# Performance work log

Measured on AMD Instinct MI355X. Metric: run time of the kernel, lower is better.

## Reference

```python
import jax, jax.numpy as jnp
import numpy as np

N = 50000      # nodes
E = 1_600_000  # edges (before self-loops)
G = 100        # graphs in batch
IN = 16        # in_channels
H1, C1 = 4, 32 # gat1 heads, per-head channels
H2, C2 = 1, 32 # gat2 heads, per-head channels
NEG_SLOPE = 0.2


def setup_inputs() -> dict:
    key = jax.random.key(0)
    ks = jax.random.split(key, 16)
    s = 0.1
    return {
        "x": jax.random.normal(ks[0], (N, IN), jnp.float32),
        "edge_index": jax.random.randint(ks[1], (2, E), 0, N, dtype=jnp.int64),
        "batch": jnp.sort(jax.random.randint(ks[2], (N,), 0, G, dtype=jnp.int64)),
        # GATConv 1: lin (no bias), att_src/att_dst, output bias (concat -> H1*C1)
        "W1": jax.random.normal(ks[3], (IN, H1 * C1), jnp.float32) * s,
        "att_src1": jax.random.normal(ks[4], (H1, C1), jnp.float32) * s,
        "att_dst1": jax.random.normal(ks[5], (H1, C1), jnp.float32) * s,
        "b1": jnp.zeros((H1 * C1,), jnp.float32),
        # GATConv 2
        "W2": jax.random.normal(ks[6], (H1 * C1, H2 * C2), jnp.float32) * s,
        "att_src2": jax.random.normal(ks[7], (H2, C2), jnp.float32) * s,
        "att_dst2": jax.random.normal(ks[8], (H2, C2), jnp.float32) * s,
        "b2": jnp.zeros((H2 * C2,), jnp.float32),
        # MLP head: Linear(32,64) -> ReLU -> Linear(64,1)
        "Wh1": jax.random.normal(ks[9], (C2, 64), jnp.float32) * s,
        "bh1": jnp.zeros((64,), jnp.float32),
        "Wh2": jax.random.normal(ks[10], (64, 1), jnp.float32) * s,
        "bh2": jnp.zeros((1,), jnp.float32),
    }


def gat_conv(x, src, dst, W, a_src, a_dst, bias, heads, ch):
    """PyG GATConv (self-loops already included in src/dst), eval mode."""
    n = x.shape[0]
    h = (x @ W).reshape(n, heads, ch)                 # [N,H,C]
    # per-node attention logits, then gather per edge
    a_s = jnp.einsum('nhc,hc->nh', h, a_src)          # [N,H]
    a_d = jnp.einsum('nhc,hc->nh', h, a_dst)
    e = jax.nn.leaky_relu(a_s[src] + a_d[dst], NEG_SLOPE)  # [E,H]
    # segment softmax over incoming edges of each destination node
    m = jax.ops.segment_max(e, dst, num_segments=n)   # [N,H]
    ex = jnp.exp(e - m[dst])
    denom = jax.ops.segment_sum(ex, dst, num_segments=n)
    alpha = ex / (denom[dst] + 1e-16)                 # [E,H]
    # weighted scatter-aggregate of source features
    out = jax.ops.segment_sum(alpha[:, :, None] * h[src], dst, num_segments=n)
    return out.reshape(n, heads * ch) + bias


def reference(x, edge_index, batch, W1, att_src1, att_dst1, b1,
              W2, att_src2, att_dst2, b2, Wh1, bh1, Wh2, bh2):
    n = x.shape[0]
    loops = jnp.arange(n, dtype=edge_index.dtype)
    src = jnp.concatenate([edge_index[0], loops])
    dst = jnp.concatenate([edge_index[1], loops])

    h = jax.nn.elu(gat_conv(x, src, dst, W1, att_src1, att_dst1, b1, H1, C1))
    h = jax.nn.elu(gat_conv(h, src, dst, W2, att_src2, att_dst2, b2, H2, C2))

    # global mean pool by graph id
    sums = jax.ops.segment_sum(h, batch, num_segments=G)          # [G,C2]
    cnts = jax.ops.segment_sum(jnp.ones((n,), h.dtype), batch, num_segments=G)
    pooled = sums / jnp.maximum(cnts, 1.0)[:, None]

    out = jax.nn.relu(pooled @ Wh1 + bh1) @ Wh2 + bh2             # [G,1]
    return out
```

## Files before the change

### kernel.cpp

```cpp
#include <hip/hip_runtime.h>
#include <hip/hip_fp16.h>
#include <math.h>

#define IN_CH 16
#define HC1 128
#define NH1 4
#define C2 32
#define HID 64
#define NEG 0.2f
#define CAP 10240
#define CHUNK 4096

__device__ __forceinline__ float lrelu_exp_fast(float z) {
    float lr = fmaxf(z, NEG * z);
    return __expf(lr);
}

__device__ __forceinline__ void fma_mix_lo(float& acc, int hpack, float w) {
    asm("v_fma_mix_f32 %0, %1, %2, %0 op_sel:[0,0,0] op_sel_hi:[1,0,0]"
        : "+v"(acc) : "v"(hpack), "v"(w));
}
__device__ __forceinline__ void fma_mix_hi(float& acc, int hpack, float w) {
    asm("v_fma_mix_f32 %0, %1, %2, %0 op_sel:[1,0,0] op_sel_hi:[1,0,0]"
        : "+v"(acc) : "v"(hpack), "v"(w));
}

__global__ void k_front(const int* __restrict__ ei, int E, int N, int nchunk,
                        int* __restrict__ cursors, int* __restrict__ buckets,
                        const float* __restrict__ x, const float2* __restrict__ W1v,
                        const float2* __restrict__ att_s2, const float2* __restrict__ att_d2,
                        __half2* __restrict__ h1h, float* __restrict__ as1, float* __restrict__ ad1) {
    int bid = blockIdx.x;
    if (bid < nchunk) {
        __shared__ int cnt[256];
        __shared__ int base[256];
        __shared__ int pos[256];
        int t = threadIdx.x;
        int c0 = bid * CHUNK;
        int M = E + N;
        cnt[t] = 0;
        pos[t] = 0;
        __syncthreads();
        int srcv[16], dstv[16];
#pragma unroll
        for (int k = 0; k < 16; ++k) {
            int i = c0 + k * 256 + t;
            int s = -1, d = -1;
            if (i < M) {
                if (i < E) { s = ei[i]; d = ei[E + i]; }
                else       { s = d = i - E; }
                atomicAdd(&cnt[d >> 8], 1);
            }
            srcv[k] = s; dstv[k] = d;
        }
        __syncthreads();
        if (cnt[t] > 0) base[t] = atomicAdd(&cursors[t], cnt[t]);
        __syncthreads();
#pragma unroll
        for (int k = 0; k < 16; ++k) {
            int d = dstv[k];
            if (d >= 0) {
                int b = d >> 8;
                int p = base[b] + atomicAdd(&pos[b], 1);
                buckets[b * CAP + p] = (srcv[k] << 8) | (d & 255);
            }
        }
    } else {
        int wave = threadIdx.x >> 6;
        int lane = threadIdx.x & 63;
        int n = (bid - nchunk) * 4 + wave;
        if (n >= N) return;
        float xv = x[n * IN_CH + (lane & 15)];
        float ax = 0.f, ay = 0.f;
#pragma unroll
        for (int k = 0; k < IN_CH; ++k) {
            float xk = __shfl(xv, k, 16);
            float2 w = W1v[k * 64 + lane];
            ax += xk * w.x;
            ay += xk * w.y;
        }
        h1h[(size_t)n * 64 + lane] = __floats2half2_rn(ax, ay);
        float2 s2 = att_s2[lane], d2 = att_d2[lane];
        float vs = ax * s2.x + ay * s2.y;
        float vd = ax * d2.x + ay * d2.y;
#pragma unroll
        for (int o = 1; o < 16; o <<= 1) {
            vs += __shfl_xor(vs, o, 64);
            vd += __shfl_xor(vd, o, 64);
        }
        if ((lane & 15) == 0) {
            as1[n * NH1 + (lane >> 4)] = vs;
            ad1[n * NH1 + (lane >> 4)] = vd;
        }
    }
}

__global__ void k_build(const int* __restrict__ buckets, const int* __restrict__ cursors,
                        int N, int M,
                        int* __restrict__ offsets, int* __restrict__ elist) {
    __shared__ int sc[256];
    __shared__ int deg[256];
    __shared__ int cur[256];
    int b = blockIdx.x, t = threadIdx.x;
    int cv = cursors[t];
    sc[t] = cv;
    __syncthreads();
    for (int o = 1; o < 256; o <<= 1) {
        int a = (t >= o) ? sc[t - o] : 0;
        __syncthreads();
        sc[t] += a;
        __syncthreads();
    }
    int cnt = cursors[b];
    int gbase = sc[b] - cnt;
    int n0 = b << 8;
    const int* bk = buckets + b * CAP;
    deg[t] = 0;
    if (b == 0 && t == 0) offsets[N] = M;
    __syncthreads();
    for (int i = t; i < cnt; i += 256) atomicAdd(&deg[bk[i] & 255], 1);
    __syncthreads();
    int v = deg[t];
    sc[t] = v;
    __syncthreads();
    for (int o = 1; o < 256; o <<= 1) {
        int a = (t >= o) ? sc[t - o] : 0;
        __syncthreads();
        sc[t] += a;
        __syncthreads();
    }
    int excl = sc[t] - v;
    cur[t] = excl;
    if (n0 + t < N) offsets[n0 + t] = gbase + excl;
    __syncthreads();
    for (int i = t; i < cnt; i += 256) {
        int e = bk[i];
        int p = atomicAdd(&cur[e & 255], 1);
        elist[gbase + p] = e >> 8;
    }
}

__global__ void k_agg1(const int* __restrict__ offsets, const int* __restrict__ elist,
                       const char* __restrict__ as1b, const float* __restrict__ ad1,
                       const char* __restrict__ h1b, const float* __restrict__ b1,
                       int N, float4* __restrict__ out1q) {
    int wave = threadIdx.x >> 6;
    int lane = threadIdx.x & 63;
    int n = blockIdx.x * 4 + wave;
    if (n >= N) return;
    int slot = lane >> 4, chunk = lane & 15, head = chunk >> 2;
    int lo = offsets[n], hi = offsets[n + 1];
    float adh = ad1[n * NH1 + head];
    unsigned coff = (unsigned)(chunk << 4);
    unsigned hoff = (unsigned)(head << 2);
    float acc[8];
#pragma unroll
    for (int j = 0; j < 8; ++j) acc[j] = 0.f;
    float sumw = 0.f;
    for (int e0 = lo; e0 < hi; e0 += 16) {
        unsigned s[4]; bool ok[4]; float z[4]; float4 v[4]; float w[4];
#pragma unroll
        for (int u = 0; u < 4; ++u) {
            int ee = e0 + 4 * u + slot;
            ok[u] = ee < hi;
            s[u] = (unsigned)elist[ok[u] ? ee : lo];
        }
#pragma unroll
        for (int u = 0; u < 4; ++u) {
            z[u] = *(const float*)(as1b + (s[u] * 16u + hoff));
            v[u] = *(const float4*)(h1b + (s[u] * 256u + coff));
        }
#pragma unroll
        for (int u = 0; u < 4; ++u)
            w[u] = ok[u] ? lrelu_exp_fast(z[u] + adh) : 0.f;
#pragma unroll
        for (int u = 0; u < 4; ++u) {
            const int* hp = (const int*)&v[u];
            fma_mix_lo(acc[0], hp[0], w[u]); fma_mix_hi(acc[1], hp[0], w[u]);
            fma_mix_lo(acc[2], hp[1], w[u]); fma_mix_hi(acc[3], hp[1], w[u]);
            fma_mix_lo(acc[4], hp[2], w[u]); fma_mix_hi(acc[5], hp[2], w[u]);
            fma_mix_lo(acc[6], hp[3], w[u]); fma_mix_hi(acc[7], hp[3], w[u]);
            sumw += w[u];
        }
    }
#pragma unroll
    for (int j = 0; j < 8; ++j) {
        acc[j] += __shfl_xor(acc[j], 16, 64);
        acc[j] += __shfl_xor(acc[j], 32, 64);
    }
    sumw += __shfl_xor(sumw, 16, 64);
    sumw += __shfl_xor(sumw, 32, 64);
    if (slot == 0) {
        float inv = 1.f / (sumw + 1e-16f);
        float4 ba = ((const float4*)b1)[2 * chunk];
        float4 bb = ((const float4*)b1)[2 * chunk + 1];
        float o[8];
        o[0] = acc[0] * inv + ba.x; o[1] = acc[1] * inv + ba.y;
        o[2] = acc[2] * inv + ba.z; o[3] = acc[3] * inv + ba.w;
        o[4] = acc[4] * inv + bb.x; o[5] = acc[5] * inv + bb.y;
        o[6] = acc[6] * inv + bb.z; o[7] = acc[7] * inv + bb.w;
#pragma unroll
        for (int j = 0; j < 8; ++j) o[j] = o[j] > 0.f ? o[j] : expm1f(o[j]);
        float4 pk;
        __half2* ph = (__half2*)&pk;
        ph[0] = __floats2half2_rn(o[0], o[1]);
        ph[1] = __floats2half2_rn(o[2], o[3]);
        ph[2] = __floats2half2_rn(o[4], o[5]);
        ph[3] = __floats2half2_rn(o[6], o[7]);
        out1q[(size_t)n * 16 + chunk] = pk;
    }
}

#define TN 64
__global__ void k_lin2(const __half2* __restrict__ out1h, const float* __restrict__ W2,
                       const float* __restrict__ att_s, const float* __restrict__ att_d,
                       int N, __half2* __restrict__ h2h, float* __restrict__ as2, float* __restrict__ ad2) {
    __shared__ float sx[TN][HC1 + 1];
    __shared__ float sw[HC1][C2];
    int t = threadIdx.x;
    int base = blockIdx.x * TN;
    int lim = (N - base) * HC1;
    for (int i = t * 4; i < HC1 * C2; i += 1024) {
        float4 v = *(const float4*)(W2 + i);
        sw[i >> 5][i & 31] = v.x;
        sw[i >> 5][(i & 31) + 1] = v.y;
        sw[i >> 5][(i & 31) + 2] = v.z;
        sw[i >> 5][(i & 31) + 3] = v.w;
    }
    for (int i = t * 4; i < TN * HC1; i += 1024) {
        float2 a = make_float2(0.f, 0.f), b = make_float2(0.f, 0.f);
        if (i < lim) {
            size_t idx = ((size_t)base * HC1 + i) >> 1;
            a = __half22float2(out1h[idx]);
            b = __half22float2(out1h[idx + 1]);
        }
        int nn = i >> 7, kk = i & 127;
        sx[nn][kk] = a.x; sx[nn][kk + 1] = a.y; sx[nn][kk + 2] = b.x; sx[nn][kk + 3] = b.y;
    }
    __syncthreads();
    int nloc = t >> 2;
    int c0 = (t & 3) * 8;
    float acc[8];
#pragma unroll
    for (int j = 0; j < 8; ++j) acc[j] = 0.f;
#pragma unroll 4
    for (int k = 0; k < HC1; ++k) {
        float xv = sx[nloc][k];
        float4 wa = *(float4*)&sw[k][c0];
        float4 wb = *(float4*)&sw[k][c0 + 4];
        acc[0] += xv * wa.x; acc[1] += xv * wa.y; acc[2] += xv * wa.z; acc[3] += xv * wa.w;
        acc[4] += xv * wb.x; acc[5] += xv * wb.y; acc[6] += xv * wb.z; acc[7] += xv * wb.w;
    }
    int n = base + nloc;
    if (n < N) {
#pragma unroll
        for (int j = 0; j < 4; ++j)
            h2h[(size_t)n * 16 + (c0 >> 1) + j] = __floats2half2_rn(acc[2 * j], acc[2 * j + 1]);
        float ps = 0.f, pd = 0.f;
#pragma unroll
        for (int j = 0; j < 8; ++j) {
            ps += acc[j] * att_s[c0 + j];
            pd += acc[j] * att_d[c0 + j];
        }
        ps += __shfl_down(ps, 1, 64); ps += __shfl_down(ps, 2, 64);
        pd += __shfl_down(pd, 1, 64); pd += __shfl_down(pd, 2, 64);
        if ((t & 3) == 0) { as2[n] = ps; ad2[n] = pd; }
    }
}

__global__ void k_agg2(const int* __restrict__ offsets, const int* __restrict__ elist,
                       const char* __restrict__ as2b, const float* __restrict__ ad2,
                       const char* __restrict__ h2b, const float* __restrict__ b2,
                       int N, float* __restrict__ out2) {
    int wave = threadIdx.x >> 6;
    int lane = threadIdx.x & 63;
    int n = blockIdx.x * 4 + wave;
    if (n >= N) return;
    int slot = lane >> 2, chunk = lane & 3;
    int lo = offsets[n], hi = offsets[n + 1];
    float ad = ad2[n];
    unsigned coff = (unsigned)(chunk << 4);
    float acc[8];
#pragma unroll
    for (int j = 0; j < 8; ++j) acc[j] = 0.f;
    float sumw = 0.f;
    for (int e0 = lo; e0 < hi; e0 += 32) {
        unsigned s[2]; bool ok[2]; float z[2]; float4 v[2]; float w[2];
#pragma unroll
        for (int u = 0; u < 2; ++u) {
            int ee = e0 + 16 * u + slot;
            ok[u] = ee < hi;
            s[u] = (unsigned)elist[ok[u] ? ee : lo];
        }
#pragma unroll
        for (int u = 0; u < 2; ++u) {
            z[u] = *(const float*)(as2b + (s[u] * 4u));
            v[u] = *(const float4*)(h2b + (s[u] * 64u + coff));
        }
#pragma unroll
        for (int u = 0; u < 2; ++u)
            w[u] = ok[u] ? lrelu_exp_fast(z[u] + ad) : 0.f;
#pragma unroll
        for (int u = 0; u < 2; ++u) {
            const int* hp = (const int*)&v[u];
            fma_mix_lo(acc[0], hp[0], w[u]); fma_mix_hi(acc[1], hp[0], w[u]);
            fma_mix_lo(acc[2], hp[1], w[u]); fma_mix_hi(acc[3], hp[1], w[u]);
            fma_mix_lo(acc[4], hp[2], w[u]); fma_mix_hi(acc[5], hp[2], w[u]);
            fma_mix_lo(acc[6], hp[3], w[u]); fma_mix_hi(acc[7], hp[3], w[u]);
            sumw += w[u];
        }
    }
#pragma unroll
    for (int j = 0; j < 8; ++j) {
        acc[j] += __shfl_xor(acc[j], 4, 64);
        acc[j] += __shfl_xor(acc[j], 8, 64);
        acc[j] += __shfl_xor(acc[j], 16, 64);
        acc[j] += __shfl_xor(acc[j], 32, 64);
    }
    sumw += __shfl_xor(sumw, 4, 64);
    sumw += __shfl_xor(sumw, 8, 64);
    sumw += __shfl_xor(sumw, 16, 64);
    sumw += __shfl_xor(sumw, 32, 64);
    if (slot == 0) {
        float inv = 1.f / (sumw + 1e-16f);
        float4 ba = ((const float4*)b2)[2 * chunk];
        float4 bb = ((const float4*)b2)[2 * chunk + 1];
        float o[8];
        o[0] = acc[0] * inv + ba.x; o[1] = acc[1] * inv + ba.y;
        o[2] = acc[2] * inv + ba.z; o[3] = acc[3] * inv + ba.w;
        o[4] = acc[4] * inv + bb.x; o[5] = acc[5] * inv + bb.y;
        o[6] = acc[6] * inv + bb.z; o[7] = acc[7] * inv + bb.w;
#pragma unroll
        for (int j = 0; j < 8; ++j) o[j] = o[j] > 0.f ? o[j] : expm1f(o[j]);
        float* dst = out2 + (size_t)n * C2 + 8 * chunk;
        *(float4*)dst = make_float4(o[0], o[1], o[2], o[3]);
        *(float4*)(dst + 4) = make_float4(o[4], o[5], o[6], o[7]);
    }
}

__global__ void k_pool(const float* __restrict__ out2, const int* __restrict__ batch,
                       int N, const float* __restrict__ Wh1, const float* __restrict__ bh1,
                       const float* __restrict__ Wh2, const float* __restrict__ bh2,
                       float* __restrict__ out) {
    int g = blockIdx.x;
    int t = threadIdx.x;
    __shared__ int sb[2];
    __shared__ float pooled[C2];
    __shared__ float red[256];
    if (t < 2) {
        int target = g + t;
        int lo = 0, hi = N;
        while (lo < hi) { int mid = (lo + hi) >> 1; if (batch[mid] < target) lo = mid + 1; else hi = mid; }
        sb[t] = lo;
    }
    __syncthreads();
    int lo = sb[0], hi = sb[1];
    int c = t & 31, grp = t >> 5;
    float part = 0.f;
    for (int n = lo + grp; n < hi; n += 8) part += out2[n * C2 + c];
    red[t] = part;
    __syncthreads();
    if (t < 128) red[t] += red[t + 128];
    __syncthreads();
    if (t < 64) red[t] += red[t + 64];
    __syncthreads();
    if (t < 32) {
        red[t] += red[t + 32];
        float cnt = (float)(hi - lo);
        pooled[t] = red[t] / fmaxf(cnt, 1.f);
    }
    __syncthreads();
    float hval = 0.f;
    if (t < HID) {
        float a = bh1[t];
#pragma unroll
        for (int cc = 0; cc < C2; ++cc) a += pooled[cc] * Wh1[cc * HID + t];
        hval = fmaxf(a, 0.f) * Wh2[t];
    }
    if (t < 64) {
        for (int o = 32; o > 0; o >>= 1) hval += __shfl_down(hval, o, 64);
        if (t == 0) out[g] = hval + bh2[0];
    }
}

extern "C" void kernel_launch(void* const* d_in, const int* in_sizes, int n_in,
                              void* d_out, int out_size, void* d_ws, size_t ws_size,
                              hipStream_t stream) {
    const float* x    = (const float*)d_in[0];
    const int*   ei   = (const int*)d_in[1];
    const int*   batch= (const int*)d_in[2];
    const float* W1   = (const float*)d_in[3];
    const float* aS1  = (const float*)d_in[4];
    const float* aD1  = (const float*)d_in[5];
    const float* b1   = (const float*)d_in[6];
    const float* W2   = (const float*)d_in[7];
    const float* aS2  = (const float*)d_in[8];
    const float* aD2  = (const float*)d_in[9];
    const float* b2   = (const float*)d_in[10];
    const float* Wh1  = (const float*)d_in[11];
    const float* bh1  = (const float*)d_in[12];
    const float* Wh2  = (const float*)d_in[13];
    const float* bh2  = (const float*)d_in[14];
    float* out = (float*)d_out;

    int N = in_sizes[2];
    int E = in_sizes[1] / 2;
    int M = E + N;
    int G = out_size;
    int nbk = (N + 255) >> 8;
    int nchunk = (M + CHUNK - 1) / CHUNK;
    int nlin = (N + 3) / 4;

    char* p = (char*)d_ws;
    auto alloc = [&](size_t bytes) -> void* {
        void* r = (void*)p;
        p += (bytes + 255) & ~(size_t)255;
        return r;
    };
    __half2* h1h   = (__half2*)alloc((size_t)N * 64 * 4);
    __half2* out1h = (__half2*)alloc((size_t)N * 64 * 4);
    __half2* h2h   = (__half2*)alloc((size_t)N * 16 * 4);
    float* as1     = (float*)alloc((size_t)N * NH1 * 4);
    float* ad1     = (float*)alloc((size_t)N * NH1 * 4);
    float* as2     = (float*)alloc((size_t)N * 4);
    float* ad2     = (float*)alloc((size_t)N * 4);
    float* out2    = (float*)alloc((size_t)N * C2 * 4);
    int*   offsets = (int*)alloc((size_t)(N + 1) * 4);
    int*   elist   = (int*)alloc((size_t)M * 4);
    int*   cursors = (int*)alloc(256 * 4);
    int*   buckets = (int*)alloc((size_t)nbk * CAP * 4);

    hipMemsetAsync(cursors, 0, 256 * 4, stream);
    k_front<<<nchunk + nlin, 256, 0, stream>>>(ei, E, N, nchunk, cursors, buckets,
                                               x, (const float2*)W1, (const float2*)aS1,
                                               (const float2*)aD1, h1h, as1, ad1);
    k_build<<<nbk, 256, 0, stream>>>(buckets, cursors, N, M, offsets, elist);
    k_agg1<<<(N + 3) / 4, 256, 0, stream>>>(offsets, elist, (const char*)as1, ad1,
                                            (const char*)h1h, b1, N, (float4*)out1h);
    k_lin2<<<(N + TN - 1) / TN, 256, 0, stream>>>(out1h, W2, aS2, aD2, N, h2h, as2, ad2);
    k_agg2<<<(N + 3) / 4, 256, 0, stream>>>(offsets, elist, (const char*)as2, ad2,
                                            (const char*)h2h, b2, N, out2);
    k_pool<<<G, 256, 0, stream>>>(out2, batch, N, Wh1, bh1, Wh2, bh2, out);
}
```

Before: 279.1 us.

## Store layer-1 features head-major and split aggregation blocks per head

```diff
diff --git a/kernel.cpp b/kernel.cpp
--- a/kernel.cpp
+++ b/kernel.cpp
@@ -29,7 +29,7 @@
                         int* __restrict__ cursors, int* __restrict__ buckets,
                         const float* __restrict__ x, const float2* __restrict__ W1v,
                         const float2* __restrict__ att_s2, const float2* __restrict__ att_d2,
-                        __half2* __restrict__ h1h, float* __restrict__ as1, float* __restrict__ ad1) {
+                        __half2* __restrict__ h1s, float* __restrict__ as1s, float* __restrict__ ad1s) {
     int bid = blockIdx.x;
     if (bid < nchunk) {
         __shared__ int cnt[256];
@@ -79,7 +79,8 @@
             ax += xk * w.x;
             ay += xk * w.y;
         }
-        h1h[(size_t)n * 64 + lane] = __floats2half2_rn(ax, ay);
+        int head = lane >> 4;
+        h1s[((size_t)head * N + n) * 16 + (lane & 15)] = __floats2half2_rn(ax, ay);
         float2 s2 = att_s2[lane], d2 = att_d2[lane];
         float vs = ax * s2.x + ay * s2.y;
         float vd = ax * d2.x + ay * d2.y;
@@ -89,8 +90,8 @@
             vd += __shfl_xor(vd, o, 64);
         }
         if ((lane & 15) == 0) {
-            as1[n * NH1 + (lane >> 4)] = vs;
-            ad1[n * NH1 + (lane >> 4)] = vd;
+            as1s[(size_t)head * N + n] = vs;
+            ad1s[(size_t)head * N + n] = vd;
         }
     }
 }
@@ -141,40 +142,44 @@
 }
 
 __global__ void k_agg1(const int* __restrict__ offsets, const int* __restrict__ elist,
-                       const char* __restrict__ as1b, const float* __restrict__ ad1,
+                       const char* __restrict__ as1b, const float* __restrict__ ad1s,
                        const char* __restrict__ h1b, const float* __restrict__ b1,
-                       int N, float4* __restrict__ out1q) {
+                       int N, int nblk, char* __restrict__ out1b) {
+    int bid = blockIdx.x;
+    unsigned head = (unsigned)bid / (unsigned)nblk;
+    int nb = bid - (int)head * nblk;
     int wave = threadIdx.x >> 6;
     int lane = threadIdx.x & 63;
-    int n = blockIdx.x * 4 + wave;
+    int n = nb * 4 + wave;
     if (n >= N) return;
-    int slot = lane >> 4, chunk = lane & 15, head = chunk >> 2;
+    int slot = lane >> 2, c4 = lane & 3;
     int lo = offsets[n], hi = offsets[n + 1];
-    float adh = ad1[n * NH1 + head];
-    unsigned coff = (unsigned)(chunk << 4);
-    unsigned hoff = (unsigned)(head << 2);
+    const char* ab = as1b + (size_t)head * N * 4;
+    const char* hb = h1b + (size_t)head * N * 64;
+    float adh = ad1s[(size_t)head * N + n];
+    unsigned coff = (unsigned)(c4 << 4);
     float acc[8];
 #pragma unroll
     for (int j = 0; j < 8; ++j) acc[j] = 0.f;
     float sumw = 0.f;
-    for (int e0 = lo; e0 < hi; e0 += 16) {
-        unsigned s[4]; bool ok[4]; float z[4]; float4 v[4]; float w[4];
-#pragma unroll
-        for (int u = 0; u < 4; ++u) {
-            int ee = e0 + 4 * u + slot;
+    for (int e0 = lo; e0 < hi; e0 += 32) {
+        unsigned s[2]; bool ok[2]; float z[2]; float4 v[2]; float w[2];
+#pragma unroll
+        for (int u = 0; u < 2; ++u) {
+            int ee = e0 + 16 * u + slot;
             ok[u] = ee < hi;
             s[u] = (unsigned)elist[ok[u] ? ee : lo];
         }
 #pragma unroll
-        for (int u = 0; u < 4; ++u) {
-            z[u] = *(const float*)(as1b + (s[u] * 16u + hoff));
-            v[u] = *(const float4*)(h1b + (s[u] * 256u + coff));
-        }
-#pragma unroll
-        for (int u = 0; u < 4; ++u)
+        for (int u = 0; u < 2; ++u) {
+            z[u] = *(const float*)(ab + (s[u] * 4u));
+            v[u] = *(const float4*)(hb + (s[u] * 64u + coff));
+        }
+#pragma unroll
+        for (int u = 0; u < 2; ++u)
             w[u] = ok[u] ? lrelu_exp_fast(z[u] + adh) : 0.f;
 #pragma unroll
-        for (int u = 0; u < 4; ++u) {
+        for (int u = 0; u < 2; ++u) {
             const int* hp = (const int*)&v[u];
             fma_mix_lo(acc[0], hp[0], w[u]); fma_mix_hi(acc[1], hp[0], w[u]);
             fma_mix_lo(acc[2], hp[1], w[u]); fma_mix_hi(acc[3], hp[1], w[u]);
@@ -185,29 +190,31 @@
     }
 #pragma unroll
     for (int j = 0; j < 8; ++j) {
+        acc[j] += __shfl_xor(acc[j], 4, 64);
+        acc[j] += __shfl_xor(acc[j], 8, 64);
         acc[j] += __shfl_xor(acc[j], 16, 64);
         acc[j] += __shfl_xor(acc[j], 32, 64);
     }
+    sumw += __shfl_xor(sumw, 4, 64);
+    sumw += __shfl_xor(sumw, 8, 64);
     sumw += __shfl_xor(sumw, 16, 64);
     sumw += __shfl_xor(sumw, 32, 64);
     if (slot == 0) {
         float inv = 1.f / (sumw + 1e-16f);
-        float4 ba = ((const float4*)b1)[2 * chunk];
-        float4 bb = ((const float4*)b1)[2 * chunk + 1];
+        const float* bp = b1 + head * 32 + c4 * 8;
         float o[8];
-        o[0] = acc[0] * inv + ba.x; o[1] = acc[1] * inv + ba.y;
-        o[2] = acc[2] * inv + ba.z; o[3] = acc[3] * inv + ba.w;
-        o[4] = acc[4] * inv + bb.x; o[5] = acc[5] * inv + bb.y;
-        o[6] = acc[6] * inv + bb.z; o[7] = acc[7] * inv + bb.w;
-#pragma unroll
-        for (int j = 0; j < 8; ++j) o[j] = o[j] > 0.f ? o[j] : expm1f(o[j]);
+#pragma unroll
+        for (int j = 0; j < 8; ++j) {
+            float val = acc[j] * inv + bp[j];
+            o[j] = val > 0.f ? val : expm1f(val);
+        }
         float4 pk;
         __half2* ph = (__half2*)&pk;
         ph[0] = __floats2half2_rn(o[0], o[1]);
         ph[1] = __floats2half2_rn(o[2], o[3]);
         ph[2] = __floats2half2_rn(o[4], o[5]);
         ph[3] = __floats2half2_rn(o[6], o[7]);
-        out1q[(size_t)n * 16 + chunk] = pk;
+        *(float4*)(out1b + ((size_t)n * 256 + head * 64 + coff)) = pk;
     }
 }
 
@@ -410,6 +417,7 @@
     int nbk = (N + 255) >> 8;
     int nchunk = (M + CHUNK - 1) / CHUNK;
     int nlin = (N + 3) / 4;
+    int nblk = (N + 3) / 4;
 
     char* p = (char*)d_ws;
     auto alloc = [&](size_t bytes) -> void* {
@@ -417,11 +425,11 @@
         p += (bytes + 255) & ~(size_t)255;
         return r;
     };
-    __half2* h1h   = (__half2*)alloc((size_t)N * 64 * 4);
+    __half2* h1s   = (__half2*)alloc((size_t)N * 64 * 4);
     __half2* out1h = (__half2*)alloc((size_t)N * 64 * 4);
     __half2* h2h   = (__half2*)alloc((size_t)N * 16 * 4);
-    float* as1     = (float*)alloc((size_t)N * NH1 * 4);
-    float* ad1     = (float*)alloc((size_t)N * NH1 * 4);
+    float* as1s    = (float*)alloc((size_t)N * NH1 * 4);
+    float* ad1s    = (float*)alloc((size_t)N * NH1 * 4);
     float* as2     = (float*)alloc((size_t)N * 4);
     float* ad2     = (float*)alloc((size_t)N * 4);
     float* out2    = (float*)alloc((size_t)N * C2 * 4);
@@ -433,10 +441,10 @@
     hipMemsetAsync(cursors, 0, 256 * 4, stream);
     k_front<<<nchunk + nlin, 256, 0, stream>>>(ei, E, N, nchunk, cursors, buckets,
                                                x, (const float2*)W1, (const float2*)aS1,
-                                               (const float2*)aD1, h1h, as1, ad1);
+                                               (const float2*)aD1, h1s, as1s, ad1s);
     k_build<<<nbk, 256, 0, stream>>>(buckets, cursors, N, M, offsets, elist);
-    k_agg1<<<(N + 3) / 4, 256, 0, stream>>>(offsets, elist, (const char*)as1, ad1,
-                                            (const char*)h1h, b1, N, (float4*)out1h);
+    k_agg1<<<4 * nblk, 256, 0, stream>>>(offsets, elist, (const char*)as1s, ad1s,
+                                         (const char*)h1s, b1, N, nblk, (char*)out1h);
     k_lin2<<<(N + TN - 1) / TN, 256, 0, stream>>>(out1h, W2, aS2, aD2, N, h2h, as2, ad2);
     k_agg2<<<(N + 3) / 4, 256, 0, stream>>>(offsets, elist, (const char*)as2, ad2,
                                             (const char*)h2h, b2, N, out2);
```

Measured after the change: 366.2 us. 31.2% more time.

## Fuse layer-2 linear projection into layer-1 aggregation epilogue

Applied to the files above, without the earlier changes.

```diff
diff --git a/kernel.cpp b/kernel.cpp
--- a/kernel.cpp
+++ b/kernel.cpp
@@ -14,6 +14,9 @@
 __device__ __forceinline__ float lrelu_exp_fast(float z) {
     float lr = fmaxf(z, NEG * z);
     return __expf(lr);
+}
+__device__ __forceinline__ float elu_fast(float v) {
+    return v > 0.f ? v : __expf(v) - 1.0f;
 }
 
 __device__ __forceinline__ void fma_mix_lo(float& acc, int hpack, float w) {
@@ -143,11 +146,22 @@
 __global__ void k_agg1(const int* __restrict__ offsets, const int* __restrict__ elist,
                        const char* __restrict__ as1b, const float* __restrict__ ad1,
                        const char* __restrict__ h1b, const float* __restrict__ b1,
-                       int N, float4* __restrict__ out1q) {
-    int wave = threadIdx.x >> 6;
-    int lane = threadIdx.x & 63;
+                       const float* __restrict__ W2,
+                       const float* __restrict__ aS2v, const float* __restrict__ aD2v,
+                       int N, __half2* __restrict__ h2h,
+                       float* __restrict__ as2, float* __restrict__ ad2) {
+    __shared__ float swl[HC1][36];
+    __shared__ float sxrow[4][HC1];
+    int t = threadIdx.x;
+    for (int i = t; i < HC1 * C2; i += 256)
+        swl[i >> 5][i & 31] = W2[i];
+    __syncthreads();
+
+    int wave = t >> 6;
+    int lane = t & 63;
     int n = blockIdx.x * 4 + wave;
     if (n >= N) return;
+
     int slot = lane >> 4, chunk = lane & 15, head = chunk >> 2;
     int lo = offsets[n], hi = offsets[n + 1];
     float adh = ad1[n * NH1 + head];
@@ -194,77 +208,43 @@
         float inv = 1.f / (sumw + 1e-16f);
         float4 ba = ((const float4*)b1)[2 * chunk];
         float4 bb = ((const float4*)b1)[2 * chunk + 1];
-        float o[8];
-        o[0] = acc[0] * inv + ba.x; o[1] = acc[1] * inv + ba.y;
-        o[2] = acc[2] * inv + ba.z; o[3] = acc[3] * inv + ba.w;
-        o[4] = acc[4] * inv + bb.x; o[5] = acc[5] * inv + bb.y;
-        o[6] = acc[6] * inv + bb.z; o[7] = acc[7] * inv + bb.w;
-#pragma unroll
-        for (int j = 0; j < 8; ++j) o[j] = o[j] > 0.f ? o[j] : expm1f(o[j]);
-        float4 pk;
-        __half2* ph = (__half2*)&pk;
-        ph[0] = __floats2half2_rn(o[0], o[1]);
-        ph[1] = __floats2half2_rn(o[2], o[3]);
-        ph[2] = __floats2half2_rn(o[4], o[5]);
-        ph[3] = __floats2half2_rn(o[6], o[7]);
-        out1q[(size_t)n * 16 + chunk] = pk;
-    }
-}
-
-#define TN 64
-__global__ void k_lin2(const __half2* __restrict__ out1h, const float* __restrict__ W2,
-                       const float* __restrict__ att_s, const float* __restrict__ att_d,
-                       int N, __half2* __restrict__ h2h, float* __restrict__ as2, float* __restrict__ ad2) {
-    __shared__ float sx[TN][HC1 + 1];
-    __shared__ float sw[HC1][C2];
-    int t = threadIdx.x;
-    int base = blockIdx.x * TN;
-    int lim = (N - base) * HC1;
-    for (int i = t * 4; i < HC1 * C2; i += 1024) {
-        float4 v = *(const float4*)(W2 + i);
-        sw[i >> 5][i & 31] = v.x;
-        sw[i >> 5][(i & 31) + 1] = v.y;
-        sw[i >> 5][(i & 31) + 2] = v.z;
-        sw[i >> 5][(i & 31) + 3] = v.w;
-    }
-    for (int i = t * 4; i < TN * HC1; i += 1024) {
-        float2 a = make_float2(0.f, 0.f), b = make_float2(0.f, 0.f);
-        if (i < lim) {
-            size_t idx = ((size_t)base * HC1 + i) >> 1;
-            a = __half22float2(out1h[idx]);
-            b = __half22float2(out1h[idx + 1]);
-        }
-        int nn = i >> 7, kk = i & 127;
-        sx[nn][kk] = a.x; sx[nn][kk + 1] = a.y; sx[nn][kk + 2] = b.x; sx[nn][kk + 3] = b.y;
-    }
-    __syncthreads();
-    int nloc = t >> 2;
-    int c0 = (t & 3) * 8;
-    float acc[8];
-#pragma unroll
-    for (int j = 0; j < 8; ++j) acc[j] = 0.f;
-#pragma unroll 4
-    for (int k = 0; k < HC1; ++k) {
-        float xv = sx[nloc][k];
-        float4 wa = *(float4*)&sw[k][c0];
-        float4 wb = *(float4*)&sw[k][c0 + 4];
-        acc[0] += xv * wa.x; acc[1] += xv * wa.y; acc[2] += xv * wa.z; acc[3] += xv * wa.w;
-        acc[4] += xv * wb.x; acc[5] += xv * wb.y; acc[6] += xv * wb.z; acc[7] += xv * wb.w;
-    }
-    int n = base + nloc;
-    if (n < N) {
-#pragma unroll
-        for (int j = 0; j < 4; ++j)
-            h2h[(size_t)n * 16 + (c0 >> 1) + j] = __floats2half2_rn(acc[2 * j], acc[2 * j + 1]);
-        float ps = 0.f, pd = 0.f;
-#pragma unroll
-        for (int j = 0; j < 8; ++j) {
-            ps += acc[j] * att_s[c0 + j];
-            pd += acc[j] * att_d[c0 + j];
-        }
-        ps += __shfl_down(ps, 1, 64); ps += __shfl_down(ps, 2, 64);
-        pd += __shfl_down(pd, 1, 64); pd += __shfl_down(pd, 2, 64);
-        if ((t & 3) == 0) { as2[n] = ps; ad2[n] = pd; }
+        float4 oa, ob;
+        oa.x = elu_fast(acc[0] * inv + ba.x); oa.y = elu_fast(acc[1] * inv + ba.y);
+        oa.z = elu_fast(acc[2] * inv + ba.z); oa.w = elu_fast(acc[3] * inv + ba.w);
+        ob.x = elu_fast(acc[4] * inv + bb.x); ob.y = elu_fast(acc[5] * inv + bb.y);
+        ob.z = elu_fast(acc[6] * inv + bb.z); ob.w = elu_fast(acc[7] * inv + bb.w);
+        float4* dst4 = (float4*)&sxrow[wave][chunk * 8];
+        dst4[0] = oa;
+        dst4[1] = ob;
+    }
+    __builtin_amdgcn_wave_barrier();
+
+    int c4 = (lane & 7) * 4;
+    int kh = lane >> 3;
+    float g0 = 0.f, g1 = 0.f, g2 = 0.f, g3 = 0.f;
+    const float* xr = &sxrow[wave][kh * 16];
+#pragma unroll
+    for (int kk4 = 0; kk4 < 4; ++kk4) {
+        float4 xv = *(const float4*)(xr + kk4 * 4);
+#pragma unroll
+        for (int j = 0; j < 4; ++j) {
+            float x1 = (j == 0) ? xv.x : (j == 1) ? xv.y : (j == 2) ? xv.z : xv.w;
+            float4 wv = *(const float4*)&swl[kh * 16 + kk4 * 4 + j][c4];
+            g0 += x1 * wv.x; g1 += x1 * wv.y; g2 += x1 * wv.z; g3 += x1 * wv.w;
+        }
+    }
+    g0 += __shfl_xor(g0, 8, 64); g0 += __shfl_xor(g0, 16, 64); g0 += __shfl_xor(g0, 32, 64);
+    g1 += __shfl_xor(g1, 8, 64); g1 += __shfl_xor(g1, 16, 64); g1 += __shfl_xor(g1, 32, 64);
+    g2 += __shfl_xor(g2, 8, 64); g2 += __shfl_xor(g2, 16, 64); g2 += __shfl_xor(g2, 32, 64);
+    g3 += __shfl_xor(g3, 8, 64); g3 += __shfl_xor(g3, 16, 64); g3 += __shfl_xor(g3, 32, 64);
+    if (lane < 8) {
+        h2h[(size_t)n * 16 + (c4 >> 1)]     = __floats2half2_rn(g0, g1);
+        h2h[(size_t)n * 16 + (c4 >> 1) + 1] = __floats2half2_rn(g2, g3);
+        float ps = g0 * aS2v[c4] + g1 * aS2v[c4 + 1] + g2 * aS2v[c4 + 2] + g3 * aS2v[c4 + 3];
+        float pd = g0 * aD2v[c4] + g1 * aD2v[c4 + 1] + g2 * aD2v[c4 + 2] + g3 * aD2v[c4 + 3];
+        ps += __shfl_xor(ps, 1, 64); ps += __shfl_xor(ps, 2, 64); ps += __shfl_xor(ps, 4, 64);
+        pd += __shfl_xor(pd, 1, 64); pd += __shfl_xor(pd, 2, 64); pd += __shfl_xor(pd, 4, 64);
+        if (lane == 0) { as2[n] = ps; ad2[n] = pd; }
     }
 }
 
@@ -326,12 +306,10 @@
         float4 ba = ((const float4*)b2)[2 * chunk];
         float4 bb = ((const float4*)b2)[2 * chunk + 1];
         float o[8];
-        o[0] = acc[0] * inv + ba.x; o[1] = acc[1] * inv + ba.y;
-        o[2] = acc[2] * inv + ba.z; o[3] = acc[3] * inv + ba.w;
-        o[4] = acc[4] * inv + bb.x; o[5] = acc[5] * inv + bb.y;
-        o[6] = acc[6] * inv + bb.z; o[7] = acc[7] * inv + bb.w;
-#pragma unroll
-        for (int j = 0; j < 8; ++j) o[j] = o[j] > 0.f ? o[j] : expm1f(o[j]);
+        o[0] = elu_fast(acc[0] * inv + ba.x); o[1] = elu_fast(acc[1] * inv + ba.y);
+        o[2] = elu_fast(acc[2] * inv + ba.z); o[3] = elu_fast(acc[3] * inv + ba.w);
+        o[4] = elu_fast(acc[4] * inv + bb.x); o[5] = elu_fast(acc[5] * inv + bb.y);
+        o[6] = elu_fast(acc[6] * inv + bb.z); o[7] = elu_fast(acc[7] * inv + bb.w);
         float* dst = out2 + (size_t)n * C2 + 8 * chunk;
         *(float4*)dst = make_float4(o[0], o[1], o[2], o[3]);
         *(float4*)(dst + 4) = make_float4(o[4], o[5], o[6], o[7]);
@@ -418,7 +396,6 @@
         return r;
     };
     __half2* h1h   = (__half2*)alloc((size_t)N * 64 * 4);
-    __half2* out1h = (__half2*)alloc((size_t)N * 64 * 4);
     __half2* h2h   = (__half2*)alloc((size_t)N * 16 * 4);
     float* as1     = (float*)alloc((size_t)N * NH1 * 4);
     float* ad1     = (float*)alloc((size_t)N * NH1 * 4);
@@ -436,8 +413,8 @@
                                                (const float2*)aD1, h1h, as1, ad1);
     k_build<<<nbk, 256, 0, stream>>>(buckets, cursors, N, M, offsets, elist);
     k_agg1<<<(N + 3) / 4, 256, 0, stream>>>(offsets, elist, (const char*)as1, ad1,
-                                            (const char*)h1h, b1, N, (float4*)out1h);
-    k_lin2<<<(N + TN - 1) / TN, 256, 0, stream>>>(out1h, W2, aS2, aD2, N, h2h, as2, ad2);
+                                            (const char*)h1h, b1, W2, aS2, aD2,
+                                            N, h2h, as2, ad2);
     k_agg2<<<(N + 3) / 4, 256, 0, stream>>>(offsets, elist, (const char*)as2, ad2,
                                             (const char*)h2h, b2, N, out2);
     k_pool<<<G, 256, 0, stream>>>(out2, batch, N, Wh1, bh1, Wh2, bh2, out);
```

Result: no change. 275.2 us (-1.4%).
